# Kernel optimization log

Measured on AMD Instinct MI355X. Metric: run time of the kernel, lower is better.

Reference implementation:

```python
import jax, jax.numpy as jnp
import numpy as np

CHEB_K = 3
DIM_IN = 2
HIDDEN = 64
EMBED_DIM = 10
NODE_NUM = 2048
BATCH = 32


def _gconv(x, supports, W, b, cheb_k=CHEB_K):
    # Chebyshev graph conv applied directly to x (equivalent to building
    # T_k(A) matrices then applying: T_k(A) x = 2 A T_{k-1}(A) x - T_{k-2}(A) x).
    xs = [x, jnp.einsum('nm,bmc->bnc', supports, x)]
    for _ in range(2, cheb_k):
        xs.append(2.0 * jnp.einsum('nm,bmc->bnc', supports, xs[-1]) - xs[-2])
    x_g = jnp.concatenate(xs, axis=-1)          # [B, N, cheb_k*C]
    return jnp.einsum('bni,io->bno', x_g, W) + b


def setup_inputs() -> dict:
    key = jax.random.key(0)
    ks = jax.random.split(key, 7)
    c_in = DIM_IN + HIDDEN                       # 66
    # xavier_normal-ish scale for weights
    def xavier(k, fan_in, fan_out):
        std = float(np.sqrt(2.0 / (fan_in + fan_out)))
        return jax.random.normal(k, (fan_in, fan_out), dtype=jnp.float32) * std
    return {
        'x': jax.random.normal(ks[0], (BATCH, NODE_NUM, DIM_IN), dtype=jnp.float32),
        'state': jax.random.normal(ks[1], (BATCH, NODE_NUM, HIDDEN), dtype=jnp.float32),
        'node_embeddings': jax.random.normal(ks[2], (NODE_NUM, EMBED_DIM), dtype=jnp.float32),
        'W_gate': xavier(ks[3], CHEB_K * c_in, 2 * HIDDEN),
        'b_gate': jnp.zeros((2 * HIDDEN,), dtype=jnp.float32),
        'W_update': xavier(ks[4], CHEB_K * c_in, HIDDEN),
        'b_update': jnp.zeros((HIDDEN,), dtype=jnp.float32),
    }


def reference(x, state, node_embeddings, W_gate, b_gate, W_update, b_update):
    # adaptive adjacency: softmax(relu(E E^T), axis=1)
    logits = jnp.einsum('nc,mc->nm', node_embeddings, node_embeddings)
    supports = jax.nn.softmax(jax.nn.relu(logits), axis=1)   # [N, N]

    input_and_state = jnp.concatenate([x, state], axis=-1)   # [B, N, dim_in+hidden]
    z_r = jax.nn.sigmoid(_gconv(input_and_state, supports, W_gate, b_gate))
    z, r = jnp.split(z_r, 2, axis=-1)                        # each [B, N, hidden]
    candidate = jnp.concatenate([x, z * state], axis=-1)
    hc = jnp.tanh(_gconv(candidate, supports, W_update, b_update))
    h = r * state + (1.0 - r) * hc
    return h
```

## Files before the change

### kernel.cpp

```cpp
#include <hip/hip_runtime.h>


typedef __bf16 bf16x8 __attribute__((ext_vector_type(8)));
typedef __bf16 bf16x4 __attribute__((ext_vector_type(4)));
typedef float  f32x4  __attribute__((ext_vector_type(4)));

#define GLB(p) ((__attribute__((address_space(1))) void*)(void*)(p))
#define LDS(p) ((__attribute__((address_space(3))) void*)(p))

__global__ __launch_bounds__(256, 2)
void prologue_kernel(const float* __restrict__ E, __bf16* __restrict__ S,
                     const float* __restrict__ Wg, __bf16* __restrict__ WTg,
                     const float* __restrict__ Wu, __bf16* __restrict__ WTu,
                     const float* __restrict__ x, const float* __restrict__ st,
                     __bf16* __restrict__ T, __bf16* __restrict__ G) {
    const int bid = blockIdx.x;
    const int t = threadIdx.x;
    __shared__ float Ls[66 * 129];
    if (bid >= 2304) {
        const int rb = bid - 2304;
        const int b  = rb >> 4;
        const int n0 = (rb & 15) << 7;
        const size_t mb = (size_t)b * 2048 + n0;
        if (t < 128) {
            const float2 v = *(const float2*)&x[(mb + t) * 2];
            Ls[t] = v.x;
            Ls[129 + t] = v.y;
        }
#pragma unroll
        for (int r = 0; r < 8; ++r) {
            const int task = r * 256 + t;
            const int q = task & 15, n = task >> 4;
            f32x4 v = *(const f32x4*)&st[(mb + n) * 64 + q * 4];
            const int base = (2 + q * 4) * 129 + n;
#pragma unroll
            for (int j = 0; j < 4; ++j) Ls[base + j * 129] = v[j];
        }
        __syncthreads();
#pragma unroll
        for (int r = 0; r < 5; ++r) {
            const int task = r * 256 + t;
            if (task < 1056) {
                const int c = task >> 4, seg = task & 15;
                const float* src = &Ls[c * 129 + seg * 8];
                bf16x8 o;
#pragma unroll
                for (int j = 0; j < 8; ++j) o[j] = (__bf16)src[j];
                *(bf16x8*)&T[(size_t)(b * 66 + c) * 2048 + n0 + seg * 8] = o;
            }
        }
        {
            const int n = t & 127, half = t >> 7;
            const size_t grow = ((size_t)(b * 2048 + n0 + n)) * 256;
            for (int oct = half * 5; oct < (half ? 9 : 5); ++oct) {
                bf16x8 o8;
#pragma unroll
                for (int j = 0; j < 8; ++j) {
                    const int cc = oct * 8 + j;
                    o8[j] = (cc < 66) ? (__bf16)Ls[cc * 129 + n] : (__bf16)0.f;
                }
                *(bf16x8*)&G[grow + oct * 8] = o8;
            }
        }
        return;
    }
    if (bid >= 2048) {
        const float* W = (bid < 2176) ? Wg : Wu;
        __bf16* WT = (bid < 2176) ? WTg : WTu;
        const int Nout = (bid < 2176) ? 128 : 64;
        const int id = (bid - ((bid < 2176) ? 2048 : 2176)) * 256 + t;
        const int o = id >> 8, k = id & 255;
        const int jj = (k >= 144) ? 2 : (k >= 72 ? 1 : 0);
        const int cc = k - 72 * jj;
        const bool ok = (o < Nout) && (cc < 66) && (k < 216);
        float v = 0.f;
        if (ok) {
            if (jj == 0)      v = W[(size_t)cc * Nout + o] - W[(size_t)(132 + cc) * Nout + o];
            else if (jj == 1) v = W[(size_t)(66 + cc) * Nout + o];
            else              v = 2.f * W[(size_t)(132 + cc) * Nout + o];
        }
        WT[id] = (__bf16)v;
        return;
    }
    const int n = bid;
    const int l = t & 63, w = t >> 6;
    float* sm = Ls;
    float* ss = Ls + 4;
    float en[10];
#pragma unroll
    for (int i = 0; i < 10; ++i) en[i] = E[n * 10 + i];
    float vals[8];
    float mx = 0.f;
#pragma unroll
    for (int q = 0; q < 8; ++q) {
        const int m = q * 256 + t;
        const float* em = E + (size_t)m * 10;
        float d = 0.f;
#pragma unroll
        for (int i = 0; i < 10; ++i) d += en[i] * em[i];
        d = fmaxf(d, 0.f);
        vals[q] = d;
        mx = fmaxf(mx, d);
    }
#pragma unroll
    for (int off = 32; off; off >>= 1) mx = fmaxf(mx, __shfl_xor(mx, off));
    if (l == 0) sm[w] = mx;
    __syncthreads();
    mx = fmaxf(fmaxf(sm[0], sm[1]), fmaxf(sm[2], sm[3]));
    float sum = 0.f;
#pragma unroll
    for (int q = 0; q < 8; ++q) { vals[q] = __expf(vals[q] - mx); sum += vals[q]; }
#pragma unroll
    for (int off = 32; off; off >>= 1) sum += __shfl_xor(sum, off);
    if (l == 0) ss[w] = sum;
    __syncthreads();
    sum = ss[0] + ss[1] + ss[2] + ss[3];
    const float inv = 1.f / sum;
#pragma unroll
    for (int q = 0; q < 8; ++q) S[(size_t)n * 2048 + q * 256 + t] = (__bf16)(vals[q] * inv);
}

__global__ __launch_bounds__(256, 3)
void gemm_pipe(const __bf16* __restrict__ A, int lda,
               const __bf16* __restrict__ Bt, int ldb,
               int K, int epi, int swz,
               __bf16* __restrict__ outT,
               float* __restrict__ outF, const float* __restrict__ bias,
               const __bf16* __restrict__ zrI,
               const float* __restrict__ state,
               __bf16* __restrict__ Gout, int gsec) {
    __shared__ __align__(16) __bf16 As[2][128 * 64];
    __shared__ __align__(16) __bf16 Bs[2][64 * 64];
    int mt, ct;
    if (swz) { mt = blockIdx.x & 15; ct = blockIdx.x >> 4; }
    else     { mt = blockIdx.x;      ct = blockIdx.y; }
    const int m0 = mt * 128, c0 = ct * 64;
    const int t = threadIdx.x;
    const int l = t & 63, w = t >> 6;
    const int wr = w >> 1, wc = w & 1;
    const int lm = l & 15, kq = l >> 4, lm7 = lm & 7;
    const int sr = l >> 3;
    const int gsw = (l & 7) ^ sr;

    f32x4 acc[4][2];
#pragma unroll
    for (int i = 0; i < 4; ++i)
#pragma unroll
        for (int j = 0; j < 2; ++j) acc[i][j] = (f32x4)0.f;

    const __bf16* Asrc = A  + (size_t)(m0 + w * 8 + sr) * lda + gsw * 8;
    const __bf16* Bsrc = Bt + (size_t)(c0 + w * 8 + sr) * ldb + gsw * 8;
    const int dstA = w * 512 + l * 8;

    auto stage = [&](int buf, int k0) {
#pragma unroll
        for (int q = 0; q < 4; ++q)
            __builtin_amdgcn_global_load_lds(GLB(Asrc + (size_t)q * 32 * lda + k0),
                                             LDS(&As[buf][q * 2048 + dstA]), 16, 0, 0);
#pragma unroll
        for (int q = 0; q < 2; ++q)
            __builtin_amdgcn_global_load_lds(GLB(Bsrc + (size_t)q * 32 * ldb + k0),
                                             LDS(&Bs[buf][q * 2048 + dstA]), 16, 0, 0);
    };
    auto compute = [&](int buf) {
        const __bf16* Ab = &As[buf][0];
        const __bf16* Bb = &Bs[buf][0];
#pragma unroll
        for (int ks = 0; ks < 2; ++ks) {
            const int ga = (((ks << 2) | kq) ^ lm7) << 3;
            bf16x8 af[4], bfr[2];
#pragma unroll
            for (int i = 0; i < 4; ++i)
                af[i] = *(const bf16x8*)&Ab[(wr * 64 + i * 16 + lm) * 64 + ga];
#pragma unroll
            for (int j = 0; j < 2; ++j)
                bfr[j] = *(const bf16x8*)&Bb[(wc * 32 + j * 16 + lm) * 64 + ga];
#pragma unroll
            for (int i = 0; i < 4; ++i)
#pragma unroll
                for (int j = 0; j < 2; ++j)
                    acc[i][j] = __builtin_amdgcn_mfma_f32_16x16x32_bf16(af[i], bfr[j], acc[i][j], 0, 0, 0);
        }
    };

    stage(0, 0);
    const int iters = K >> 6;
    for (int i = 0; i + 2 <= iters; i += 2) {
        stage(1, (i + 1) << 6);
        __builtin_amdgcn_sched_barrier(0);
        __builtin_amdgcn_s_waitcnt(0x0F76);
        __builtin_amdgcn_s_barrier();
        __builtin_amdgcn_sched_barrier(0);
        compute(0);
        __builtin_amdgcn_sched_barrier(0);
        __builtin_amdgcn_s_barrier();
        __builtin_amdgcn_sched_barrier(0);
        if (i + 2 < iters) {
            stage(0, (i + 2) << 6);
            __builtin_amdgcn_sched_barrier(0);
            __builtin_amdgcn_s_waitcnt(0x0F76);
        } else {
            __builtin_amdgcn_s_waitcnt(0x0F70);
        }
        __builtin_amdgcn_s_barrier();
        __builtin_amdgcn_sched_barrier(0);
        compute(1);
        __builtin_amdgcn_sched_barrier(0);
        if (i + 4 <= iters) {
            __builtin_amdgcn_s_barrier();
            __builtin_amdgcn_sched_barrier(0);
        }
    }

    const int rb0 = m0 + wr * 64 + kq * 4;
    const int cb0 = c0 + wc * 32 + lm;
#pragma unroll
    for (int i = 0; i < 4; ++i) {
        const int rbase = rb0 + i * 16;
#pragma unroll
        for (int j = 0; j < 2; ++j) {
            const int c = cb0 + j * 16;
            f32x4 v = acc[i][j];
            if (epi <= 1) {
                bf16x4 pk;
#pragma unroll
                for (int r = 0; r < 4; ++r) pk[r] = (__bf16)v[r];
                if (epi == 0)
                    *(bf16x4*)&outT[(size_t)c * 2048 + rbase] = pk;
                const int b = c / 66, cc = c - b * 66;
                const size_t gb = ((size_t)(b * 2048 + rbase)) * 256 + gsec + cc;
#pragma unroll
                for (int r = 0; r < 4; ++r) Gout[gb + (size_t)r * 256] = pk[r];
            } else {
                if (c < 64) {
                    const float bb = bias[c];
#pragma unroll
                    for (int r = 0; r < 4; ++r) {
                        const int m = rbase + r;
                        float xx = fminf(fmaxf(v[r] + bb, -15.f), 15.f);
                        float e = __expf(2.f * xx);
                        float hc = (e - 1.f) / (e + 1.f);
                        float rr = (float)zrI[(size_t)m * 64 + c];
                        float s = state[(size_t)m * 64 + c];
                        outF[(size_t)m * 64 + c] = rr * s + (1.f - rr) * hc;
                    }
                }
            }
        }
    }
}

__global__ __launch_bounds__(256, 2)
void gemm_w(const __bf16* __restrict__ A,
            const __bf16* __restrict__ Bt,
            __bf16* __restrict__ outT, const float* __restrict__ bias,
            __bf16* __restrict__ zrO,
            const float* __restrict__ state,
            __bf16* __restrict__ Gout,
            const float* __restrict__ xin) {
    __shared__ __align__(16) __bf16 As[2][128 * 64];
    __shared__ __align__(16) __bf16 Bs[2][128 * 64];
    const int m0 = blockIdx.x * 128;
    const int t = threadIdx.x;
    const int l = t & 63, w = t >> 6;
    const int wr = w >> 1, wc = w & 1;
    const int lm = l & 15, kq = l >> 4, lm7 = lm & 7;
    const int sr = l >> 3;
    const int gsw = (l & 7) ^ sr;

    f32x4 acc[4][4];
#pragma unroll
    for (int i = 0; i < 4; ++i)
#pragma unroll
        for (int j = 0; j < 4; ++j) acc[i][j] = (f32x4)0.f;

    const __bf16* Asrc = A  + (size_t)(m0 + w * 8 + sr) * 256 + gsw * 8;
    const __bf16* Bsrc = Bt + (size_t)(w * 8 + sr) * 256 + gsw * 8;
    const int dstA = w * 512 + l * 8;

    auto stage = [&](int buf, int k0) {
#pragma unroll
        for (int q = 0; q < 4; ++q)
            __builtin_amdgcn_global_load_lds(GLB(Asrc + (size_t)q * 32 * 256 + k0),
                                             LDS(&As[buf][q * 2048 + dstA]), 16, 0, 0);
#pragma unroll
        for (int q = 0; q < 4; ++q)
            __builtin_amdgcn_global_load_lds(GLB(Bsrc + (size_t)q * 32 * 256 + k0),
                                             LDS(&Bs[buf][q * 2048 + dstA]), 16, 0, 0);
    };
    auto compute = [&](int buf) {
        const __bf16* Ab = &As[buf][0];
        const __bf16* Bb = &Bs[buf][0];
#pragma unroll
        for (int ks = 0; ks < 2; ++ks) {
            const int ga = (((ks << 2) | kq) ^ lm7) << 3;
            bf16x8 af[4], bfr[4];
#pragma unroll
            for (int i = 0; i < 4; ++i)
                af[i] = *(const bf16x8*)&Ab[(wr * 64 + i * 16 + lm) * 64 + ga];
#pragma unroll
            for (int j = 0; j < 4; ++j)
                bfr[j] = *(const bf16x8*)&Bb[(wc * 64 + j * 16 + lm) * 64 + ga];
#pragma unroll
            for (int i = 0; i < 4; ++i)
#pragma unroll
                for (int j = 0; j < 4; ++j)
                    acc[i][j] = __builtin_amdgcn_mfma_f32_16x16x32_bf16(af[i], bfr[j], acc[i][j], 0, 0, 0);
        }
    };

    stage(0, 0);
    const int iters = 4;
    for (int i = 0; i + 2 <= iters; i += 2) {
        stage(1, (i + 1) << 6);
        __builtin_amdgcn_sched_barrier(0);
        __builtin_amdgcn_s_waitcnt(0x0F78);
        __builtin_amdgcn_s_barrier();
        __builtin_amdgcn_sched_barrier(0);
        compute(0);
        __builtin_amdgcn_sched_barrier(0);
        __builtin_amdgcn_s_barrier();
        __builtin_amdgcn_sched_barrier(0);
        if (i + 2 < iters) {
            stage(0, (i + 2) << 6);
            __builtin_amdgcn_sched_barrier(0);
            __builtin_amdgcn_s_waitcnt(0x0F78);
        } else {
            __builtin_amdgcn_s_waitcnt(0x0F70);
        }
        __builtin_amdgcn_s_barrier();
        __builtin_amdgcn_sched_barrier(0);
        compute(1);
        __builtin_amdgcn_sched_barrier(0);
        if (i + 4 <= iters) {
            __builtin_amdgcn_s_barrier();
            __builtin_amdgcn_sched_barrier(0);
        }
    }

    const int rb0 = m0 + wr * 64 + kq * 4;
    const int cb0 = wc * 64 + lm;
#pragma unroll
    for (int i = 0; i < 4; ++i) {
        const int rbase = rb0 + i * 16;
#pragma unroll
        for (int j = 0; j < 4; ++j) {
            const int c = cb0 + j * 16;
            f32x4 v = acc[i][j];
            const float bb = bias[c];
            if (c < 64) {
                const int b = rbase >> 11, n = rbase & 2047;
                bf16x4 pk;
#pragma unroll
                for (int r = 0; r < 4; ++r) {
                    float xx = fminf(fmaxf(v[r] + bb, -30.f), 30.f);
                    const float z = 1.f / (1.f + __expf(-xx));
                    const float sv = state[(size_t)(rbase + r) * 64 + c];
                    pk[r] = (__bf16)(z * sv);
                    Gout[((size_t)(rbase + r)) * 256 + 2 + c] = pk[r];
                }
                *(bf16x4*)&outT[(size_t)(b * 66 + 2 + c) * 2048 + n] = pk;
            } else {
#pragma unroll
                for (int r = 0; r < 4; ++r) {
                    float xx = fminf(fmaxf(v[r] + bb, -30.f), 30.f);
                    zrO[(size_t)(rbase + r) * 64 + (c - 64)] = (__bf16)(1.f / (1.f + __expf(-xx)));
                }
            }
        }
    }
    if (t < 128) {
        const int m = m0 + t;
        const int b = m >> 11, n = m & 2047;
        const float2 vx = *(const float2*)&xin[(size_t)m * 2];
        outT[(size_t)(b * 66) * 2048 + n]     = (__bf16)vx.x;
        outT[(size_t)(b * 66 + 1) * 2048 + n] = (__bf16)vx.y;
        Gout[(size_t)m * 256 + 0] = (__bf16)vx.x;
        Gout[(size_t)m * 256 + 1] = (__bf16)vx.y;
#pragma unroll
        for (int cc = 66; cc < 72; ++cc) Gout[(size_t)m * 256 + cc] = (__bf16)0.f;
    }
}

extern "C" void kernel_launch(void* const* d_in, const int* in_sizes, int n_in,
                              void* d_out, int out_size, void* d_ws, size_t ws_size,
                              hipStream_t stream) {
    (void)in_sizes; (void)n_in; (void)out_size; (void)ws_size;
    const float* x  = (const float*)d_in[0];
    const float* st = (const float*)d_in[1];
    const float* E  = (const float*)d_in[2];
    const float* Wg = (const float*)d_in[3];
    const float* bg = (const float*)d_in[4];
    const float* Wu = (const float*)d_in[5];
    const float* bu = (const float*)d_in[6];
    float* out = (float*)d_out;

    char* p = (char*)d_ws;
    __bf16* S   = (__bf16*)p; p += (size_t)2048 * 2048 * 2;
    __bf16* T0  = (__bf16*)p; p += (size_t)2112 * 2048 * 2;
    __bf16* T1  = (__bf16*)p; p += (size_t)2112 * 2048 * 2;
    __bf16* Gg  = (__bf16*)p; p += (size_t)65536 * 256 * 2;
    __bf16* Gu  = (__bf16*)p; p += (size_t)65536 * 256 * 2;
    __bf16* ZR  = (__bf16*)p; p += (size_t)65536 * 64 * 2;
    __bf16* WTg = (__bf16*)p; p += 128 * 256 * 2;
    __bf16* WTu = (__bf16*)p; p += 128 * 256 * 2;

    prologue_kernel<<<2816, 256, 0, stream>>>(E, S, Wg, WTg, Wu, WTu, x, st, T0, Gg);

    gemm_pipe<<<528, 256, 0, stream>>>(S, 2048, T0, 2048, 2048, 0, 1, T1, nullptr, nullptr, nullptr, nullptr, Gg, 72);
    gemm_pipe<<<528, 256, 0, stream>>>(S, 2048, T1, 2048, 2048, 1, 1, nullptr, nullptr, nullptr, nullptr, nullptr, Gg, 144);
    gemm_w<<<512, 256, 0, stream>>>(Gg, WTg, T0, bg, ZR, st, Gu, x);

    gemm_pipe<<<528, 256, 0, stream>>>(S, 2048, T0, 2048, 2048, 0, 1, T1, nullptr, nullptr, nullptr, nullptr, Gu, 72);
    gemm_pipe<<<528, 256, 0, stream>>>(S, 2048, T1, 2048, 2048, 1, 1, nullptr, nullptr, nullptr, nullptr, nullptr, Gu, 144);
    gemm_pipe<<<dim3(512, 1), 256, 0, stream>>>(Gu, 256, WTu, 256, 256, 3, 0, nullptr, out, bu, ZR, st, nullptr, 0);
}
```

Before: 252.2 us.

## Stage GEMM epilogue through LDS for coalesced writes and reuse propagated x channels

The propagation GEMMs and gemm_w now write their bf16 results into a swizzled LDS tile and then emit 16-byte vectorized rows into the concatenated G buffer, replacing scattered 2-byte strided stores. In the update pass, T0 is laid out as 64 channels per batch without the x channels. The x-derived columns of the Chebyshev terms are copied from the gate-pass buffer instead of being recomputed, which shrinks those GEMM grids from 528 to 512 blocks. This adds an LDS round-trip, a barrier and some boundary-splitting logic in the epilogue, and it relies on the gate-pass G holding S·x at fixed offsets.

```diff
diff --git a/kernel.cpp b/kernel.cpp
--- a/kernel.cpp
+++ b/kernel.cpp
@@ -3,6 +3,7 @@
 
 typedef __bf16 bf16x8 __attribute__((ext_vector_type(8)));
 typedef __bf16 bf16x4 __attribute__((ext_vector_type(4)));
+typedef __bf16 bf16x2 __attribute__((ext_vector_type(2)));
 typedef float  f32x4  __attribute__((ext_vector_type(4)));
 
 #define GLB(p) ((__attribute__((address_space(1))) void*)(void*)(p))
@@ -123,7 +124,7 @@
 __global__ __launch_bounds__(256, 3)
 void gemm_pipe(const __bf16* __restrict__ A, int lda,
                const __bf16* __restrict__ Bt, int ldb,
-               int K, int epi, int swz,
+               int K, int epi, int swz, int cmode,
                __bf16* __restrict__ outT,
                float* __restrict__ outF, const float* __restrict__ bias,
                const __bf16* __restrict__ zrI,
@@ -214,6 +215,7 @@
 
     const int rb0 = m0 + wr * 64 + kq * 4;
     const int cb0 = c0 + wc * 32 + lm;
+    __bf16* Lt = &As[0][0];
 #pragma unroll
     for (int i = 0; i < 4; ++i) {
         const int rbase = rb0 + i * 16;
@@ -227,10 +229,14 @@
                 for (int r = 0; r < 4; ++r) pk[r] = (__bf16)v[r];
                 if (epi == 0)
                     *(bf16x4*)&outT[(size_t)c * 2048 + rbase] = pk;
-                const int b = c / 66, cc = c - b * 66;
-                const size_t gb = ((size_t)(b * 2048 + rbase)) * 256 + gsec + cc;
-#pragma unroll
-                for (int r = 0; r < 4; ++r) Gout[gb + (size_t)r * 256] = pk[r];
+                const int mbL = wr * 64 + kq * 4 + i * 16;
+                const int clocb = wc * 32 + lm + j * 16;
+#pragma unroll
+                for (int r = 0; r < 4; ++r) {
+                    const int ml = mbL + r;
+                    const int swr = (ml & 7) ^ ((ml >> 3) & 7);
+                    Lt[ml * 64 + ((((clocb >> 3) ^ swr) & 7) << 3) + (clocb & 7)] = pk[r];
+                }
             } else {
                 if (c < 64) {
                     const float bb = bias[c];
@@ -243,6 +249,33 @@
                         float rr = (float)zrI[(size_t)m * 64 + c];
                         float s = state[(size_t)m * 64 + c];
                         outF[(size_t)m * 64 + c] = rr * s + (1.f - rr) * hc;
+                    }
+                }
+            }
+        }
+    }
+    if (epi <= 1) {
+        __syncthreads();
+        const int mloc = t >> 1, h = t & 1;
+        const int m = m0 + mloc;
+        const int sw = (mloc & 7) ^ ((mloc >> 3) & 7);
+#pragma unroll
+        for (int k = 0; k < 4; ++k) {
+            const int g = h * 4 + k;
+            const bf16x8 v = *(const bf16x8*)&Lt[mloc * 64 + ((g ^ sw) & 7) * 8];
+            const int c = c0 + g * 8;
+            if (cmode) {
+                const int b = c >> 6;
+                *(bf16x8*)&Gout[((size_t)(b * 2048 + m)) * 256 + gsec + 2 + (c & 63)] = v;
+            } else {
+                const int b0 = c / 66, b7 = (c + 7) / 66;
+                if (b0 == b7) {
+                    *(bf16x8*)&Gout[((size_t)(b0 * 2048 + m)) * 256 + gsec + (c - b0 * 66)] = v;
+                } else {
+#pragma unroll
+                    for (int e = 0; e < 8; ++e) {
+                        const int ce = c + e, be = ce / 66;
+                        Gout[((size_t)(be * 2048 + m)) * 256 + gsec + (ce - be * 66)] = v[e];
                     }
                 }
             }
@@ -340,6 +373,7 @@
 
     const int rb0 = m0 + wr * 64 + kq * 4;
     const int cb0 = wc * 64 + lm;
+    __bf16* Lt = &As[0][0];
 #pragma unroll
     for (int i = 0; i < 4; ++i) {
         const int rbase = rb0 + i * 16;
@@ -357,9 +391,15 @@
                     const float z = 1.f / (1.f + __expf(-xx));
                     const float sv = state[(size_t)(rbase + r) * 64 + c];
                     pk[r] = (__bf16)(z * sv);
-                    Gout[((size_t)(rbase + r)) * 256 + 2 + c] = pk[r];
-                }
-                *(bf16x4*)&outT[(size_t)(b * 66 + 2 + c) * 2048 + n] = pk;
+                }
+                *(bf16x4*)&outT[(size_t)(b * 64 + c) * 2048 + n] = pk;
+                const int mbL = wr * 64 + kq * 4 + i * 16;
+#pragma unroll
+                for (int r = 0; r < 4; ++r) {
+                    const int ml = mbL + r;
+                    const int swr = (ml & 7) ^ ((ml >> 3) & 7);
+                    Lt[ml * 64 + ((((c >> 3) ^ swr) & 7) << 3) + (c & 7)] = pk[r];
+                }
             } else {
 #pragma unroll
                 for (int r = 0; r < 4; ++r) {
@@ -369,16 +409,59 @@
             }
         }
     }
-    if (t < 128) {
-        const int m = m0 + t;
-        const int b = m >> 11, n = m & 2047;
-        const float2 vx = *(const float2*)&xin[(size_t)m * 2];
-        outT[(size_t)(b * 66) * 2048 + n]     = (__bf16)vx.x;
-        outT[(size_t)(b * 66 + 1) * 2048 + n] = (__bf16)vx.y;
-        Gout[(size_t)m * 256 + 0] = (__bf16)vx.x;
-        Gout[(size_t)m * 256 + 1] = (__bf16)vx.y;
-#pragma unroll
-        for (int cc = 66; cc < 72; ++cc) Gout[(size_t)m * 256 + cc] = (__bf16)0.f;
+    __syncthreads();
+    {
+        const int mloc = t >> 1, h = t & 1;
+        const int m = m0 + mloc;
+        const int sw = (mloc & 7) ^ ((mloc >> 3) & 7);
+        const size_t gr = (size_t)m * 256;
+        auto ldg = [&](int g) { return *(const bf16x8*)&Lt[mloc * 64 + ((g ^ sw) & 7) * 8]; };
+        if (h == 0) {
+            const float2 vx = *(const float2*)&xin[(size_t)m * 2];
+            const bf16x8 g0 = ldg(0), g1 = ldg(1), g2 = ldg(2), g3 = ldg(3), g4 = ldg(4);
+            bf16x8 o;
+            o[0] = (__bf16)vx.x; o[1] = (__bf16)vx.y;
+#pragma unroll
+            for (int e = 0; e < 6; ++e) o[2 + e] = g0[e];
+            *(bf16x8*)&Gout[gr + 0] = o;
+            o[0] = g0[6]; o[1] = g0[7];
+#pragma unroll
+            for (int e = 0; e < 6; ++e) o[2 + e] = g1[e];
+            *(bf16x8*)&Gout[gr + 8] = o;
+            o[0] = g1[6]; o[1] = g1[7];
+#pragma unroll
+            for (int e = 0; e < 6; ++e) o[2 + e] = g2[e];
+            *(bf16x8*)&Gout[gr + 16] = o;
+            o[0] = g2[6]; o[1] = g2[7];
+#pragma unroll
+            for (int e = 0; e < 6; ++e) o[2 + e] = g3[e];
+            *(bf16x8*)&Gout[gr + 24] = o;
+            o[0] = g3[6]; o[1] = g3[7];
+#pragma unroll
+            for (int e = 0; e < 6; ++e) o[2 + e] = g4[e];
+            *(bf16x8*)&Gout[gr + 32] = o;
+        } else {
+            const bf16x8 v4 = ldg(4), v5 = ldg(5), v6 = ldg(6), v7 = ldg(7);
+            bf16x8 o;
+            o[0] = v4[6]; o[1] = v4[7];
+#pragma unroll
+            for (int e = 0; e < 6; ++e) o[2 + e] = v5[e];
+            *(bf16x8*)&Gout[gr + 40] = o;
+            o[0] = v5[6]; o[1] = v5[7];
+#pragma unroll
+            for (int e = 0; e < 6; ++e) o[2 + e] = v6[e];
+            *(bf16x8*)&Gout[gr + 48] = o;
+            o[0] = v6[6]; o[1] = v6[7];
+#pragma unroll
+            for (int e = 0; e < 6; ++e) o[2 + e] = v7[e];
+            *(bf16x8*)&Gout[gr + 56] = o;
+            o[0] = v7[6]; o[1] = v7[7];
+#pragma unroll
+            for (int e = 0; e < 6; ++e) o[2 + e] = (__bf16)0.f;
+            *(bf16x8*)&Gout[gr + 64] = o;
+            *(bf16x2*)&Gout[gr + 72]  = *(const bf16x2*)&A[gr + 72];
+            *(bf16x2*)&Gout[gr + 144] = *(const bf16x2*)&A[gr + 144];
+        }
     }
 }
 
@@ -407,11 +490,11 @@
 
     prologue_kernel<<<2816, 256, 0, stream>>>(E, S, Wg, WTg, Wu, WTu, x, st, T0, Gg);
 
-    gemm_pipe<<<528, 256, 0, stream>>>(S, 2048, T0, 2048, 2048, 0, 1, T1, nullptr, nullptr, nullptr, nullptr, Gg, 72);
-    gemm_pipe<<<528, 256, 0, stream>>>(S, 2048, T1, 2048, 2048, 1, 1, nullptr, nullptr, nullptr, nullptr, nullptr, Gg, 144);
+    gemm_pipe<<<528, 256, 0, stream>>>(S, 2048, T0, 2048, 2048, 0, 1, 0, T1, nullptr, nullptr, nullptr, nullptr, Gg, 72);
+    gemm_pipe<<<528, 256, 0, stream>>>(S, 2048, T1, 2048, 2048, 1, 1, 0, nullptr, nullptr, nullptr, nullptr, nullptr, Gg, 144);
     gemm_w<<<512, 256, 0, stream>>>(Gg, WTg, T0, bg, ZR, st, Gu, x);
 
-    gemm_pipe<<<528, 256, 0, stream>>>(S, 2048, T0, 2048, 2048, 0, 1, T1, nullptr, nullptr, nullptr, nullptr, Gu, 72);
-    gemm_pipe<<<528, 256, 0, stream>>>(S, 2048, T1, 2048, 2048, 1, 1, nullptr, nullptr, nullptr, nullptr, nullptr, Gu, 144);
-    gemm_pipe<<<dim3(512, 1), 256, 0, stream>>>(Gu, 256, WTu, 256, 256, 3, 0, nullptr, out, bu, ZR, st, nullptr, 0);
+    gemm_pipe<<<512, 256, 0, stream>>>(S, 2048, T0, 2048, 2048, 0, 1, 1, T1, nullptr, nullptr, nullptr, nullptr, Gu, 72);
+    gemm_pipe<<<512, 256, 0, stream>>>(S, 2048, T1, 2048, 2048, 1, 1, 1, nullptr, nullptr, nullptr, nullptr, nullptr, Gu, 144);
+    gemm_pipe<<<dim3(512, 1), 256, 0, stream>>>(Gu, 256, WTu, 256, 256, 3, 0, 0, nullptr, out, bu, ZR, st, nullptr, 0);
 }
```

New measurement: 261.5 us. +3.7%, slower.
